# Performance work log

Measured on AMD Instinct MI355X. Metric: run time of the kernel, lower is better.

Reference implementation:

```python
import jax, jax.numpy as jnp
import numpy as np

E = 768       # embed dim
NH = 12       # heads
HD = 64       # head dim
WIN = 14      # window size
DEPTH = 12
PATCH = 16
WINDOW_IDX = (0, 1, 3, 4, 6, 7, 9, 10)
EPS = 1e-6


def layer_norm(x, w, b):
    mu = jnp.mean(x, axis=-1, keepdims=True)
    var = jnp.mean(jnp.square(x - mu), axis=-1, keepdims=True)
    return (x - mu) * jax.lax.rsqrt(var + EPS) * w + b


def get_rel_pos(size, rel_pos):
    # q_size == k_size -> direct lookup, no interpolation
    coords = jnp.arange(size)
    rel = coords[:, None] - coords[None, :] + (size - 1)
    return rel_pos[rel]  # (size, size, HD)


def attention(x, qkv_w, qkv_b, proj_w, proj_b, rel_h, rel_w):
    B, H, W, _ = x.shape
    N = H * W
    qkv = (x.reshape(B, N, E) @ qkv_w + qkv_b).reshape(B, N, 3, NH, HD)
    q = qkv[:, :, 0].transpose(0, 2, 1, 3).reshape(B * NH, N, HD)
    k = qkv[:, :, 1].transpose(0, 2, 1, 3).reshape(B * NH, N, HD)
    v = qkv[:, :, 2].transpose(0, 2, 1, 3).reshape(B * NH, N, HD)
    attn = (q * (HD ** -0.5)) @ k.transpose(0, 2, 1)  # (B*NH, N, N)
    # decomposed relative position bias
    Rh = get_rel_pos(H, rel_h)  # (H, H, HD)
    Rw = get_rel_pos(W, rel_w)  # (W, W, HD)
    r_q = q.reshape(B * NH, H, W, HD)
    rh = jnp.einsum('bhwc,hkc->bhwk', r_q, Rh)
    rw = jnp.einsum('bhwc,wkc->bhwk', r_q, Rw)
    attn = attn.reshape(B * NH, H, W, H, W) + rh[:, :, :, :, None] + rw[:, :, :, None, :]
    attn = jax.nn.softmax(attn.reshape(B * NH, N, N), axis=-1)
    out = (attn @ v).reshape(B, NH, H, W, HD).transpose(0, 2, 3, 1, 4).reshape(B, H, W, E)
    return out @ proj_w + proj_b


def window_partition(x, ws):
    B, H, W, C = x.shape
    pad_h, pad_w = (-H) % ws, (-W) % ws
    x = jnp.pad(x, ((0, 0), (0, pad_h), (0, pad_w), (0, 0)))
    Hp, Wp = H + pad_h, W + pad_w
    x = x.reshape(B, Hp // ws, ws, Wp // ws, ws, C).transpose(0, 1, 3, 2, 4, 5)
    return x.reshape(-1, ws, ws, C), (Hp, Wp)


def window_unpartition(win, ws, pad_hw, hw):
    Hp, Wp = pad_hw
    H, W = hw
    B = win.shape[0] // ((Hp // ws) * (Wp // ws))
    x = win.reshape(B, Hp // ws, Wp // ws, ws, ws, -1).transpose(0, 1, 3, 2, 4, 5)
    return x.reshape(B, Hp, Wp, -1)[:, :H, :W]


def _forward(x, patch_w, patch_b, pos_embed,
             ln1_w, ln1_b, qkv_w, qkv_b, proj_w, proj_b,
             rel_h_win, rel_w_win, rel_h_glob, rel_w_glob,
             ln2_w, ln2_b, fc1_w, fc1_b, fc2_w, fc2_b, out_w, out_b):
    # patch embed: conv 16x16 stride 16
    x = jax.lax.conv_general_dilated(
        x, patch_w, (PATCH, PATCH), 'VALID',
        dimension_numbers=('NCHW', 'OIHW', 'NCHW'))
    x = x.transpose(0, 2, 3, 1) + patch_b  # (B, H, W, C)
    x = x + pos_embed
    win_i, glob_i = 0, 0
    for i in range(DEPTH):
        shortcut = x
        h = layer_norm(x, ln1_w[i], ln1_b[i])
        if i in WINDOW_IDX:
            hw = h.shape[1:3]
            h, pad_hw = window_partition(h, WIN)
            h = attention(h, qkv_w[i], qkv_b[i], proj_w[i], proj_b[i],
                          rel_h_win[win_i], rel_w_win[win_i])
            h = window_unpartition(h, WIN, pad_hw, hw)
            win_i += 1
        else:
            h = attention(h, qkv_w[i], qkv_b[i], proj_w[i], proj_b[i],
                          rel_h_glob[glob_i], rel_w_glob[glob_i])
            glob_i += 1
        x = shortcut + h
        h = layer_norm(x, ln2_w[i], ln2_b[i])
        h = jax.nn.gelu(h @ fc1_w[i] + fc1_b[i], approximate=False) @ fc2_w[i] + fc2_b[i]
        x = x + h
    feat = x.transpose(0, 3, 1, 2)  # (B, C, H, W) == 'last_feat'
    return jnp.einsum('bchw,oc->bohw', feat, out_w) + out_b[None, :, None, None]


def setup_inputs() -> dict:
    key = jax.random.key(0)
    ks = iter(jax.random.split(key, 64))
    def n(shape, s=0.02):
        return jax.random.normal(next(ks), shape, jnp.float32) * s
    B, IMG = 2, 512
    G = IMG // PATCH  # 32
    return {
        'x': jax.random.normal(next(ks), (B, 3, IMG, IMG), jnp.float32),
        'patch_w': n((E, 3, PATCH, PATCH)),
        'patch_b': jnp.zeros((E,), jnp.float32),
        'pos_embed': n((1, G, G, E)),
        'ln1_w': jnp.ones((DEPTH, E), jnp.float32),
        'ln1_b': jnp.zeros((DEPTH, E), jnp.float32),
        'qkv_w': n((DEPTH, E, 3 * E)),
        'qkv_b': jnp.zeros((DEPTH, 3 * E), jnp.float32),
        'proj_w': n((DEPTH, E, E)),
        'proj_b': jnp.zeros((DEPTH, E), jnp.float32),
        'rel_h_win': n((8, 2 * WIN - 1, HD)),
        'rel_w_win': n((8, 2 * WIN - 1, HD)),
        'rel_h_glob': n((4, 2 * G - 1, HD)),
        'rel_w_glob': n((4, 2 * G - 1, HD)),
        'ln2_w': jnp.ones((DEPTH, E), jnp.float32),
        'ln2_b': jnp.zeros((DEPTH, E), jnp.float32),
        'fc1_w': n((DEPTH, E, 4 * E)),
        'fc1_b': jnp.zeros((DEPTH, 4 * E), jnp.float32),
        'fc2_w': n((DEPTH, 4 * E, E)),
        'fc2_b': jnp.zeros((DEPTH, E), jnp.float32),
        'out_w': n((256, E)),
        'out_b': jnp.zeros((256,), jnp.float32),
    }


def reference(x, patch_w, patch_b, pos_embed,
              ln1_w, ln1_b, qkv_w, qkv_b, proj_w, proj_b,
              rel_h_win, rel_w_win, rel_h_glob, rel_w_glob,
              ln2_w, ln2_b, fc1_w, fc1_b, fc2_w, fc2_b, out_w, out_b):
    return _forward(x, patch_w, patch_b, pos_embed,
                    ln1_w, ln1_b, qkv_w, qkv_b, proj_w, proj_b,
                    rel_h_win, rel_w_win, rel_h_glob, rel_w_glob,
                    ln2_w, ln2_b, fc1_w, fc1_b, fc2_w, fc2_b, out_w, out_b)
```

## Files before the change

kernel.cpp:

```cpp
#include <hip/hip_runtime.h>
#include <hip/hip_bf16.h>
#include <math.h>

static constexpr int E   = 768;
static constexpr int NH  = 12;
static constexpr int HD  = 64;
static constexpr int Bsz = 2;
static constexpr int G   = 32;
static constexpr int NTOK = G * G;
static constexpr int ROWS = Bsz * NTOK;
static constexpr int WS  = 14;
static constexpr int NWIN_SIDE = 3;
static constexpr int NWIN = NWIN_SIDE * NWIN_SIDE;
static constexpr int BW  = Bsz * NWIN;
static constexpr int NW  = WS * WS;
static constexpr int WROWS = BW * NW;
static constexpr int WIN_MASK = 0x6DB;

typedef __attribute__((ext_vector_type(8))) short short8;
typedef __attribute__((ext_vector_type(4))) float f32x4;
typedef unsigned short ushort_t;

__device__ __forceinline__ unsigned short f2bf(float x) {
  union { float f; unsigned u; } v; v.f = x;
  unsigned r = v.u + 0x7fffu + ((v.u >> 16) & 1u);
  return (unsigned short)(r >> 16);
}
__device__ __forceinline__ float bf2f(unsigned short h) {
  union { unsigned u; float f; } v; v.u = ((unsigned)h) << 16;
  return v.f;
}

__device__ __forceinline__ void glds16(const void* g, void* l) {
  __builtin_amdgcn_global_load_lds(
      (const __attribute__((address_space(1))) unsigned*)g,
      (__attribute__((address_space(3))) unsigned*)l, 16, 0, 0);
}

__global__ __launch_bounds__(256) void ln_kernel(
    const float* __restrict__ in, const float* __restrict__ w,
    const float* __restrict__ b, ushort_t* __restrict__ out) {
  const int wave = threadIdx.x >> 6, lane = threadIdx.x & 63;
  const int row = blockIdx.x * 4 + wave;
  const float4* r4 = (const float4*)(in + (size_t)row * E);
  float4 v[3];
  v[0] = r4[lane]; v[1] = r4[lane + 64]; v[2] = r4[lane + 128];
  float s = 0.f, s2 = 0.f;
#pragma unroll
  for (int i = 0; i < 3; i++) {
    s += v[i].x + v[i].y + v[i].z + v[i].w;
    s2 += v[i].x * v[i].x + v[i].y * v[i].y + v[i].z * v[i].z + v[i].w * v[i].w;
  }
#pragma unroll
  for (int off = 1; off <= 32; off <<= 1) {
    s += __shfl_xor(s, off);
    s2 += __shfl_xor(s2, off);
  }
  const float mean = s * (1.f / E);
  const float var  = s2 * (1.f / E) - mean * mean;
  const float rs   = rsqrtf(var + 1e-6f);
  ushort_t* o = out + (size_t)row * E;
#pragma unroll
  for (int i = 0; i < 3; i++) {
    const int e0 = (lane + i * 64) * 4;
    ushort4 p;
    p.x = f2bf((v[i].x - mean) * rs * w[e0]     + b[e0]);
    p.y = f2bf((v[i].y - mean) * rs * w[e0 + 1] + b[e0 + 1]);
    p.z = f2bf((v[i].z - mean) * rs * w[e0 + 2] + b[e0 + 2]);
    p.w = f2bf((v[i].w - mean) * rs * w[e0 + 3] + b[e0 + 3]);
    *(ushort4*)&o[e0] = p;
  }
}

enum { OP_QKV = 0, OP_GELU = 1, OP_ADD = 2, OP_POS = 3, OP_HEAD = 4 };

template <int OP, int MAP>
__global__ __launch_bounds__(256) void gemm_bt(
    const ushort_t* __restrict__ A, const ushort_t* __restrict__ Bt,
    const float* __restrict__ bias, const float* __restrict__ res,
    const float* __restrict__ pos, const ushort_t* __restrict__ zbuf,
    void* __restrict__ Cp, int M, int N, int K, int ncol) {
  __shared__ ushort_t As[2][64 * 64];
  __shared__ ushort_t Bs[2][64 * 64];
  const int tid = threadIdx.x, wave = tid >> 6, lane = tid & 63;
  const int lx = lane & 15, ly = lane >> 4;

  const int nwg = gridDim.x;
  const int q = nwg >> 3, r = nwg & 7;
  const int xcd = blockIdx.x & 7, loc = blockIdx.x >> 3;
  const int wgid = ((xcd < r) ? xcd * (q + 1) : r * (q + 1) + (xcd - r) * q) + loc;
  const int brow = wgid / ncol, bcol = wgid - brow * ncol;
  const int row0 = brow * 64, col0 = bcol * 64;
  const int wm = (wave >> 1) * 32, wn = (wave & 1) * 32;
  const int rin = lane >> 3, pseg = lane & 7;
  const int lseg = pseg ^ rin;
  f32x4 acc[2][2] = {};

  const ushort_t* aptr[2];
  const ushort_t* bptr[2];
#pragma unroll
  for (int j = 0; j < 2; j++) {
    const int slot = wave * 2 + j;
    int ar = row0 + slot * 8 + rin;
    if (ar >= M) ar = M - 1;
    if (MAP == 1) {
      const int win = ar / NW, t = ar - win * NW;
      const int wy = t / WS, wx = t - wy * WS;
      const int bI = win / NWIN, wr = win - bI * NWIN;
      const int by = wr / NWIN_SIDE, bx = wr - by * NWIN_SIDE;
      const int y = by * WS + wy, x = bx * WS + wx;
      aptr[j] = (y < G && x < G)
                    ? &A[(((size_t)bI * G + y) * G + x) * E + lseg * 8]
                    : &zbuf[lseg * 8];
    } else if (MAP == 2) {
      const int bI = ar >> 10, t = ar & 1023, y = t >> 5, x = t & 31;
      const int by = y / WS, wy = y - by * WS;
      const int bx = x / WS, wx = x - bx * WS;
      const int win = bI * NWIN + by * NWIN_SIDE + bx;
      aptr[j] = &A[((size_t)win * NW + wy * WS + wx) * E + lseg * 8];
    } else {
      aptr[j] = &A[(size_t)ar * K + lseg * 8];
    }
    const int br = col0 + slot * 8 + rin;
    bptr[j] = &Bt[(size_t)br * K + lseg * 8];
  }

#pragma unroll
  for (int j = 0; j < 2; j++) {
    const int slot = wave * 2 + j;
    glds16(aptr[j], &As[0][slot * 512]);
    glds16(bptr[j], &Bs[0][slot * 512]);
  }
  __syncthreads();

  const int nt = K >> 6;
  int cur = 0;
  for (int t = 0; t < nt; t++) {
    if (t + 1 < nt) {
      const int k1 = (t + 1) << 6;
#pragma unroll
      for (int j = 0; j < 2; j++) {
        const int slot = wave * 2 + j;
        glds16(aptr[j] + k1, &As[cur ^ 1][slot * 512]);
        glds16(bptr[j] + k1, &Bs[cur ^ 1][slot * 512]);
      }
    }
#pragma unroll
    for (int kb = 0; kb < 2; kb++) {
      short8 af[2], bfm[2];
#pragma unroll
      for (int m = 0; m < 2; m++) {
        const int rr = wm + m * 16 + lx;
        af[m] = *(const short8*)&As[cur][rr * 64 + (((kb * 4 + ly) ^ (rr & 7)) * 8)];
      }
#pragma unroll
      for (int n = 0; n < 2; n++) {
        const int rr = wn + n * 16 + lx;
        bfm[n] = *(const short8*)&Bs[cur][rr * 64 + (((kb * 4 + ly) ^ (rr & 7)) * 8)];
      }
      __builtin_amdgcn_s_setprio(1);
#pragma unroll
      for (int m = 0; m < 2; m++)
#pragma unroll
        for (int n = 0; n < 2; n++)
          acc[m][n] = __builtin_amdgcn_mfma_f32_16x16x32_bf16(af[m], bfm[n], acc[m][n], 0, 0, 0);
      __builtin_amdgcn_s_setprio(0);
    }
    __syncthreads();
    cur ^= 1;
  }

#pragma unroll
  for (int m = 0; m < 2; m++) {
#pragma unroll
    for (int r4 = 0; r4 < 4; r4++) {
      const int gr = row0 + wm + m * 16 + ly * 4 + r4;
      if (gr >= M) continue;
#pragma unroll
      for (int n = 0; n < 2; n++) {
        const int gc = col0 + wn + n * 16 + lx;
        float v = acc[m][n][r4] + bias[gc];
        if (OP == OP_GELU) v = 0.5f * v * (1.f + erff(v * 0.70710678118654752f));
        if (OP == OP_ADD)  v += res[(size_t)gr * N + gc];
        if (OP == OP_POS)  v += pos[(size_t)(gr & 1023) * N + gc];
        if (OP == OP_QKV || OP == OP_GELU)
          ((ushort_t*)Cp)[(size_t)gr * N + gc] = f2bf(v);
        else if (OP == OP_HEAD)
          ((float*)Cp)[(((size_t)(gr >> 10) * 256 + gc) << 10) | (gr & 1023)] = v;
        else
          ((float*)Cp)[(size_t)gr * N + gc] = v;
      }
    }
  }
}

__global__ __launch_bounds__(128) void attn_mfma(
    const ushort_t* __restrict__ qkv, ushort_t* __restrict__ out,
    const float* __restrict__ relh, const float* __restrict__ relw,
    int Hd, int Wd) {
  const int Ntok = Hd * Wd;
  __shared__ ushort_t smem[11392];
  ushort_t* Ks   = smem;
  ushort_t* Vst  = smem + 2048;
  ushort_t* Ps   = smem + 4608;
  ushort_t* Qs   = smem;
  ushort_t* RelS = smem + 2048;
  ushort_t* Th   = smem + 6144;
  ushort_t* Tw   = smem + 8256;
  ushort_t* khw  = smem + 10368;

  const int tid = threadIdx.x, wave = tid >> 6, lane = tid & 63;
  const int lx = lane & 15, ly = lane >> 4;
  const int bh = blockIdx.y, b = bh / NH, nh = bh % NH;
  const int q0 = blockIdx.x * 32;
  const size_t base = (size_t)b * Ntok * 2304 + nh * 64;

#pragma unroll
  for (int i = 0; i < 2; i++) {
    const int fv = i * 128 + tid;
    const int row = fv >> 3, dv8 = (fv & 7) * 8;
    const int qq = q0 + row;
    short8 v = {};
    if (qq < Ntok) v = *(const short8*)&qkv[base + (size_t)qq * 2304 + dv8];
    *(short8*)&Qs[(row * 64 + dv8) ^ ((row & 7) << 3)] = v;
  }
  for (int k = tid; k < 1024; k += 128) {
    const int kc = min(k, Ntok - 1);
    const int kh = kc / Wd;
    khw[k] = (ushort_t)((kh << 8) | (kc - kh * Wd));
  }
  __syncthreads();

  short8 qa[2];
  {
    const int row = wave * 16 + lx;
#pragma unroll
    for (int kb = 0; kb < 2; kb++)
      qa[kb] = *(const short8*)&Qs[(row * 64 + kb * 32 + ly * 8) ^ ((row & 7) << 3)];
  }
  int qh_r[4], qw_r[4];
#pragma unroll
  for (int r = 0; r < 4; r++) {
    const int qq = q0 + wave * 16 + ly * 4 + r;
    const int qc = min(qq, Ntok - 1);
    qh_r[r] = qc / Wd;
    qw_r[r] = qc - qh_r[r] * Wd;
  }

  for (int t = 0; t < 2; t++) {
    const float* rel = t ? relw : relh;
    const int TR = t ? (2 * Wd - 1) : (2 * Hd - 1);
    __syncthreads();
#pragma unroll
    for (int i = 0; i < 4; i++) {
      const int fv = i * 128 + tid;
      const int row = fv >> 3, c8 = (fv & 7) * 8;
      short8 v = {};
      if (row < TR) {
        const float* rp = &rel[(size_t)row * 64 + c8];
        const float4 a = *(const float4*)rp;
        const float4 bq = *(const float4*)(rp + 4);
        v[0] = (short)f2bf(a.x);  v[1] = (short)f2bf(a.y);
        v[2] = (short)f2bf(a.z);  v[3] = (short)f2bf(a.w);
        v[4] = (short)f2bf(bq.x); v[5] = (short)f2bf(bq.y);
        v[6] = (short)f2bf(bq.z); v[7] = (short)f2bf(bq.w);
      }
      *(short8*)&RelS[(row * 64 + c8) ^ ((row & 7) << 3)] = v;
    }
    __syncthreads();
    const int NT = (TR + 15) >> 4;
    ushort_t* T = t ? Tw : Th;
    for (int nt = 0; nt < NT; nt++) {
      f32x4 a = {};
      __builtin_amdgcn_s_setprio(1);
#pragma unroll
      for (int kb = 0; kb < 2; kb++) {
        const int rrow = nt * 16 + lx;
        short8 bfv = *(const short8*)&RelS[(rrow * 64 + kb * 32 + ly * 8) ^ ((rrow & 7) << 3)];
        a = __builtin_amdgcn_mfma_f32_16x16x32_bf16(qa[kb], bfv, a, 0, 0, 0);
      }
      __builtin_amdgcn_s_setprio(0);
#pragma unroll
      for (int reg = 0; reg < 4; reg++)
        T[(wave * 16 + ly * 4 + reg) * 66 + nt * 16 + lx] = f2bf(a[reg]);
    }
  }

  f32x4 o[4] = {};
  float m_[4], l_[4];
#pragma unroll
  for (int r = 0; r < 4; r++) { m_[r] = -3e38f; l_[r] = 0.f; }

  const int nkt = (Ntok + 31) >> 5;
  const int srow = tid >> 3, c7 = tid & 7, dv8s = c7 * 8;
  const int vswz = (c7 & 3) << 3;

  short8 kpre[2], vpre[2];
#pragma unroll
  for (int i = 0; i < 2; i++) {
    const int gk = srow + i * 16;
    short8 kv = {}, vv = {};
    if (gk < Ntok) {
      kv = *(const short8*)&qkv[base + 768 + (size_t)gk * 2304 + dv8s];
      vv = *(const short8*)&qkv[base + 1536 + (size_t)gk * 2304 + dv8s];
    }
    kpre[i] = kv; vpre[i] = vv;
  }

  for (int kt = 0; kt < nkt; kt++) {
    __syncthreads();
#pragma unroll
    for (int i = 0; i < 2; i++) {
      const int row = srow + i * 16;
      *(short8*)&Ks[(row * 64 + dv8s) ^ ((row & 7) << 3)] = kpre[i];
      const int kcol = row ^ vswz;
#pragma unroll
      for (int j = 0; j < 8; j++)
        Vst[(dv8s + j) * 40 + kcol] = (ushort_t)vpre[i][j];
    }
    if (kt + 1 < nkt) {
#pragma unroll
      for (int i = 0; i < 2; i++) {
        const int gk = (kt + 1) * 32 + srow + i * 16;
        short8 kv = {}, vv = {};
        if (gk < Ntok) {
          kv = *(const short8*)&qkv[base + 768 + (size_t)gk * 2304 + dv8s];
          vv = *(const short8*)&qkv[base + 1536 + (size_t)gk * 2304 + dv8s];
        }
        kpre[i] = kv; vpre[i] = vv;
      }
    }
    __syncthreads();

    f32x4 c[2] = {};
    __builtin_amdgcn_s_setprio(1);
#pragma unroll
    for (int kb = 0; kb < 2; kb++)
#pragma unroll
      for (int ct = 0; ct < 2; ct++) {
        const int krow = ct * 16 + lx;
        short8 kf = *(const short8*)&Ks[(krow * 64 + kb * 32 + ly * 8) ^ ((krow & 7) << 3)];
        c[ct] = __builtin_amdgcn_mfma_f32_16x16x32_bf16(qa[kb], kf, c[ct], 0, 0, 0);
      }
    __builtin_amdgcn_s_setprio(0);

    const int k0a = kt * 32 + lx, k1a = k0a + 16;
    const int tv0 = khw[k0a], tv1 = khw[k1a];
    const int kh0 = tv0 >> 8, kw0 = tv0 & 255;
    const int kh1 = tv1 >> 8, kw1 = tv1 & 255;
    float pv0[4], pv1[4], mt[4];
#pragma unroll
    for (int r = 0; r < 4; r++) {
      const int trow = (wave * 16 + ly * 4 + r) * 66;
      float s0 = c[0][r] * 0.125f + bf2f(Th[trow + qh_r[r] - kh0 + Hd - 1])
               + bf2f(Tw[trow + qw_r[r] - kw0 + Wd - 1]);
      float s1 = c[1][r] * 0.125f + bf2f(Th[trow + qh_r[r] - kh1 + Hd - 1])
               + bf2f(Tw[trow + qw_r[r] - kw1 + Wd - 1]);
      if (k0a >= Ntok) s0 = -1e30f;
      if (k1a >= Ntok) s1 = -1e30f;
      pv0[r] = s0; pv1[r] = s1;
      mt[r] = fmaxf(s0, s1);
    }
    const float dmax = fmaxf(fmaxf(mt[0] - m_[0], mt[1] - m_[1]),
                             fmaxf(mt[2] - m_[2], mt[3] - m_[3]));
    if (!__all(dmax <= 8.f)) {
#pragma unroll
      for (int r = 0; r < 4; r++) {
        float mr = mt[r];
#pragma unroll
        for (int off = 1; off <= 8; off <<= 1) mr = fmaxf(mr, __shfl_xor(mr, off));
        const float mn = fmaxf(m_[r], mr);
        const float sc = __expf(m_[r] - mn);
        m_[r] = mn; l_[r] *= sc;
#pragma unroll
        for (int dt = 0; dt < 4; dt++) o[dt][r] *= sc;
      }
    }
#pragma unroll
    for (int r = 0; r < 4; r++) {
      const float p0 = __expf(pv0[r] - m_[r]);
      const float p1 = __expf(pv1[r] - m_[r]);
      l_[r] += p0 + p1;
      const int pb = wave * 640 + (ly * 4 + r) * 40;
      Ps[pb + lx]      = f2bf(p0);
      Ps[pb + 16 + lx] = f2bf(p1);
    }
    short8 pf = *(const short8*)&Ps[wave * 640 + lx * 40 + ly * 8];
    __builtin_amdgcn_s_setprio(1);
#pragma unroll
    for (int dt = 0; dt < 4; dt++) {
      const int drow = dt * 16 + lx;
      short8 vf = *(const short8*)&Vst[drow * 40 + ((ly * 8) ^ (((drow >> 3) & 3) << 3))];
      o[dt] = __builtin_amdgcn_mfma_f32_16x16x32_bf16(pf, vf, o[dt], 0, 0, 0);
    }
    __builtin_amdgcn_s_setprio(0);
  }

#pragma unroll
  for (int r = 0; r < 4; r++) {
#pragma unroll
    for (int off = 1; off <= 8; off <<= 1) l_[r] += __shfl_xor(l_[r], off);
    const int qq = q0 + wave * 16 + ly * 4 + r;
    if (qq >= Ntok) continue;
    const float inv = 1.f / l_[r];
#pragma unroll
    for (int dt = 0; dt < 4; dt++)
      out[((size_t)b * Ntok + qq) * E + nh * 64 + dt * 16 + lx] = f2bf(o[dt][r] * inv);
  }
}

__global__ __launch_bounds__(256) void im2col(const float* __restrict__ x,
                                              ushort_t* __restrict__ out) {
  const int blk = blockIdx.x;
  const int b = blk >> 10, t = blk & 1023, gy = t >> 5, gx = t & 31;
  for (int k = threadIdx.x; k < 768; k += 256) {
    const int ci = k >> 8, rem = k & 255, py = rem >> 4, px = rem & 15;
    out[(size_t)blk * 768 + k] =
        f2bf(x[(((size_t)b * 3 + ci) * 512 + gy * 16 + py) * 512 + gx * 16 + px]);
  }
}

__global__ __launch_bounds__(256) void prep_wt(
    const float* __restrict__ qkvw, const float* __restrict__ projw,
    const float* __restrict__ fc1w, const float* __restrict__ fc2w,
    ushort_t* __restrict__ wq, ushort_t* __restrict__ wp,
    ushort_t* __restrict__ w1, ushort_t* __restrict__ w2) {
  __shared__ float tile[32][33];
  const int blk = blockIdx.x;
  const float* W; ushort_t* Wt; int Kd, Nd, tn, tk;
  if (blk < 1728)      { W = qkvw;  Wt = wq; Kd = 768;  Nd = 2304; tn = blk % 72;          tk = blk / 72; }
  else if (blk < 2304) { W = projw; Wt = wp; Kd = 768;  Nd = 768;  tn = (blk - 1728) % 24; tk = (blk - 1728) / 24; }
  else if (blk < 4608) { W = fc1w;  Wt = w1; Kd = 768;  Nd = 3072; tn = (blk - 2304) % 96; tk = (blk - 2304) / 96; }
  else                 { W = fc2w;  Wt = w2; Kd = 3072; Nd = 768;  tn = (blk - 4608) % 24; tk = (blk - 4608) / 24; }
  const int k0 = tk * 32, n0 = tn * 32;
  const int c = threadIdx.x & 31, r8 = threadIdx.x >> 5;
#pragma unroll
  for (int i = 0; i < 4; i++) {
    const int kr = i * 8 + r8;
    tile[kr][c] = W[(size_t)(k0 + kr) * Nd + n0 + c];
  }
  __syncthreads();
#pragma unroll
  for (int i = 0; i < 4; i++) {
    const int nr = i * 8 + r8;
    Wt[(size_t)(n0 + nr) * Kd + k0 + c] = f2bf(tile[c][nr]);
  }
}

__global__ __launch_bounds__(256) void cast_bf16(const float* __restrict__ in,
                                                 ushort_t* __restrict__ out, int n) {
  const int idx = (blockIdx.x * 256 + threadIdx.x) * 4;
  if (idx + 3 < n) {
    const float4 v = *(const float4*)&in[idx];
    ushort4 p;
    p.x = f2bf(v.x); p.y = f2bf(v.y); p.z = f2bf(v.z); p.w = f2bf(v.w);
    *(ushort4*)&out[idx] = p;
  }
}

__global__ __launch_bounds__(256) void zinit(ushort_t* __restrict__ z) {
  z[blockIdx.x * 256 + threadIdx.x] = 0;
}

extern "C" void kernel_launch(void* const* d_in, const int* in_sizes, int n_in,
                              void* d_out, int out_size, void* d_ws, size_t ws_size,
                              hipStream_t stream) {
  const float* x_in     = (const float*)d_in[0];
  const float* patch_w  = (const float*)d_in[1];
  const float* patch_b  = (const float*)d_in[2];
  const float* pos_emb  = (const float*)d_in[3];
  const float* ln1_w    = (const float*)d_in[4];
  const float* ln1_b    = (const float*)d_in[5];
  const float* qkv_w    = (const float*)d_in[6];
  const float* qkv_b    = (const float*)d_in[7];
  const float* proj_w   = (const float*)d_in[8];
  const float* proj_b   = (const float*)d_in[9];
  const float* rel_h_w  = (const float*)d_in[10];
  const float* rel_w_w  = (const float*)d_in[11];
  const float* rel_h_g  = (const float*)d_in[12];
  const float* rel_w_g  = (const float*)d_in[13];
  const float* ln2_w    = (const float*)d_in[14];
  const float* ln2_b    = (const float*)d_in[15];
  const float* fc1_w    = (const float*)d_in[16];
  const float* fc1_b    = (const float*)d_in[17];
  const float* fc2_w    = (const float*)d_in[18];
  const float* fc2_b    = (const float*)d_in[19];
  const float* out_w    = (const float*)d_in[20];
  const float* out_b    = (const float*)d_in[21];
  float* outp = (float*)d_out;

  float* xbuf = (float*)d_ws;
  ushort_t* hb16    = (ushort_t*)(xbuf + (size_t)ROWS * E);
  ushort_t* qkv16   = hb16 + (size_t)ROWS * E;
  ushort_t* attnw16 = qkv16 + (size_t)WROWS * 3 * E;
  ushort_t* wtbuf   = attnw16 + (size_t)WROWS * E;
  ushort_t* wq = wtbuf;
  ushort_t* wp = wq + 2304 * 768;
  ushort_t* w1 = wp + 768 * 768;
  ushort_t* w2 = w1 + 3072 * 768;
  ushort_t* zbuf = wtbuf + (size_t)9216 * 768;
  ushort_t* imb16 = hb16;
  ushort_t* h1b16 = qkv16;
  ushort_t* pwT16 = wtbuf;
  ushort_t* headW16 = wtbuf;

  zinit<<<4, 256, 0, stream>>>(zbuf);

  cast_bf16<<<576, 256, 0, stream>>>(patch_w, pwT16, 768 * 768);
  im2col<<<ROWS, 256, 0, stream>>>(x_in, imb16);
  gemm_bt<OP_POS, 0><<<12 * 32, 256, 0, stream>>>(
      imb16, pwT16, patch_b, nullptr, pos_emb, nullptr, xbuf, ROWS, E, E, 12);

  int win_i = 0, glob_i = 0;
  for (int i = 0; i < 12; i++) {
    const bool is_win = (WIN_MASK >> i) & 1;

    prep_wt<<<6912, 256, 0, stream>>>(
        qkv_w + (size_t)i * E * 3 * E, proj_w + (size_t)i * E * E,
        fc1_w + (size_t)i * E * 4 * E, fc2_w + (size_t)i * 4 * E * E,
        wq, wp, w1, w2);

    ln_kernel<<<ROWS / 4, 256, 0, stream>>>(xbuf, ln1_w + i * E, ln1_b + i * E, hb16);

    if (is_win) {
      gemm_bt<OP_QKV, 1><<<36 * 56, 256, 0, stream>>>(
          hb16, wq, qkv_b + i * 3 * E, nullptr, nullptr, zbuf, qkv16,
          WROWS, 3 * E, E, 36);
      attn_mfma<<<dim3(7, BW * NH), 128, 0, stream>>>(
          qkv16, attnw16, rel_h_w + (size_t)win_i * (2 * WS - 1) * HD,
          rel_w_w + (size_t)win_i * (2 * WS - 1) * HD, WS, WS);
      win_i++;
    } else {
      gemm_bt<OP_QKV, 0><<<36 * 32, 256, 0, stream>>>(
          hb16, wq, qkv_b + i * 3 * E, nullptr, nullptr, nullptr, qkv16,
          ROWS, 3 * E, E, 36);
      attn_mfma<<<dim3(32, Bsz * NH), 128, 0, stream>>>(
          qkv16, attnw16, rel_h_g + (size_t)glob_i * (2 * G - 1) * HD,
          rel_w_g + (size_t)glob_i * (2 * G - 1) * HD, G, G);
      glob_i++;
    }

    if (is_win)
      gemm_bt<OP_ADD, 2><<<12 * 32, 256, 0, stream>>>(
          attnw16, wp, proj_b + i * E, xbuf, nullptr, nullptr, xbuf,
          ROWS, E, E, 12);
    else
      gemm_bt<OP_ADD, 0><<<12 * 32, 256, 0, stream>>>(
          attnw16, wp, proj_b + i * E, xbuf, nullptr, nullptr, xbuf,
          ROWS, E, E, 12);

    ln_kernel<<<ROWS / 4, 256, 0, stream>>>(xbuf, ln2_w + i * E, ln2_b + i * E, hb16);
    gemm_bt<OP_GELU, 0><<<48 * 32, 256, 0, stream>>>(
        hb16, w1, fc1_b + i * 4 * E, nullptr, nullptr, nullptr, h1b16,
        ROWS, 4 * E, E, 48);
    gemm_bt<OP_ADD, 0><<<12 * 32, 256, 0, stream>>>(
        h1b16, w2, fc2_b + i * E, xbuf, nullptr, nullptr, xbuf,
        ROWS, E, 4 * E, 12);
  }

  cast_bf16<<<192, 256, 0, stream>>>(out_w, headW16, 256 * 768);
  cast_bf16<<<1536, 256, 0, stream>>>(xbuf, hb16, ROWS * E);
  gemm_bt<OP_HEAD, 0><<<4 * 32, 256, 0, stream>>>(
      hb16, headW16, out_b, nullptr, nullptr, nullptr, outp, ROWS, 256, E, 4);
}
```

Baseline: 1.834 ms.

## Run QKV GEMM on unpadded tokens and gather windows inside attention; batch weight prep

```diff
diff --git a/kernel.cpp b/kernel.cpp
--- a/kernel.cpp
+++ b/kernel.cpp
@@ -14,7 +14,6 @@
 static constexpr int NWIN = NWIN_SIDE * NWIN_SIDE;
 static constexpr int BW  = Bsz * NWIN;
 static constexpr int NW  = WS * WS;
-static constexpr int WROWS = BW * NW;
 static constexpr int WIN_MASK = 0x6DB;
 
 typedef __attribute__((ext_vector_type(8))) short short8;
@@ -74,12 +73,12 @@
 
 enum { OP_QKV = 0, OP_GELU = 1, OP_ADD = 2, OP_POS = 3, OP_HEAD = 4 };
 
-template <int OP, int MAP>
+template <int OP>
 __global__ __launch_bounds__(256) void gemm_bt(
     const ushort_t* __restrict__ A, const ushort_t* __restrict__ Bt,
     const float* __restrict__ bias, const float* __restrict__ res,
-    const float* __restrict__ pos, const ushort_t* __restrict__ zbuf,
-    void* __restrict__ Cp, int M, int N, int K, int ncol) {
+    const float* __restrict__ pos, void* __restrict__ Cp,
+    int M, int N, int K, int ncol) {
   __shared__ ushort_t As[2][64 * 64];
   __shared__ ushort_t Bs[2][64 * 64];
   const int tid = threadIdx.x, wave = tid >> 6, lane = tid & 63;
@@ -103,24 +102,7 @@
     const int slot = wave * 2 + j;
     int ar = row0 + slot * 8 + rin;
     if (ar >= M) ar = M - 1;
-    if (MAP == 1) {
-      const int win = ar / NW, t = ar - win * NW;
-      const int wy = t / WS, wx = t - wy * WS;
-      const int bI = win / NWIN, wr = win - bI * NWIN;
-      const int by = wr / NWIN_SIDE, bx = wr - by * NWIN_SIDE;
-      const int y = by * WS + wy, x = bx * WS + wx;
-      aptr[j] = (y < G && x < G)
-                    ? &A[(((size_t)bI * G + y) * G + x) * E + lseg * 8]
-                    : &zbuf[lseg * 8];
-    } else if (MAP == 2) {
-      const int bI = ar >> 10, t = ar & 1023, y = t >> 5, x = t & 31;
-      const int by = y / WS, wy = y - by * WS;
-      const int bx = x / WS, wx = x - bx * WS;
-      const int win = bI * NWIN + by * NWIN_SIDE + bx;
-      aptr[j] = &A[((size_t)win * NW + wy * WS + wx) * E + lseg * 8];
-    } else {
-      aptr[j] = &A[(size_t)ar * K + lseg * 8];
-    }
+    aptr[j] = &A[(size_t)ar * K + lseg * 8];
     const int br = col0 + slot * 8 + rin;
     bptr[j] = &Bt[(size_t)br * K + lseg * 8];
   }
@@ -194,10 +176,11 @@
   }
 }
 
+template <int WIN>
 __global__ __launch_bounds__(128) void attn_mfma(
     const ushort_t* __restrict__ qkv, ushort_t* __restrict__ out,
     const float* __restrict__ relh, const float* __restrict__ relw,
-    int Hd, int Wd) {
+    const float* __restrict__ qkvb, int Hd, int Wd) {
   const int Ntok = Hd * Wd;
   __shared__ ushort_t smem[11392];
   ushort_t* Ks   = smem;
@@ -211,17 +194,34 @@
 
   const int tid = threadIdx.x, wave = tid >> 6, lane = tid & 63;
   const int lx = lane & 15, ly = lane >> 4;
-  const int bh = blockIdx.y, b = bh / NH, nh = bh % NH;
+  const int bh = blockIdx.y;
+  const int nh = bh % NH;
+  int b, by = 0, bx = 0;
+  if (WIN) {
+    const int wb = bh / NH;
+    b = wb / NWIN;
+    const int wr = wb - b * NWIN;
+    by = wr / NWIN_SIDE; bx = wr - by * NWIN_SIDE;
+  } else {
+    b = bh / NH;
+  }
   const int q0 = blockIdx.x * 32;
-  const size_t base = (size_t)b * Ntok * 2304 + nh * 64;
+  const size_t base = (size_t)b * NTOK * 2304 + nh * 64;
 
 #pragma unroll
   for (int i = 0; i < 2; i++) {
     const int fv = i * 128 + tid;
     const int row = fv >> 3, dv8 = (fv & 7) * 8;
-    const int qq = q0 + row;
-    short8 v = {};
-    if (qq < Ntok) v = *(const short8*)&qkv[base + (size_t)qq * 2304 + dv8];
+    const int j2 = min(q0 + row, Ntok - 1);
+    size_t addr;
+    if (WIN) {
+      const int qh = (j2 * 2341) >> 15, qw = j2 - qh * 14;
+      const int gy = min(by * 14 + qh, G - 1), gx = min(bx * 14 + qw, G - 1);
+      addr = base + (size_t)(gy * G + gx) * 2304 + dv8;
+    } else {
+      addr = base + (size_t)j2 * 2304 + dv8;
+    }
+    short8 v = *(const short8*)&qkv[addr];
     *(short8*)&Qs[(row * 64 + dv8) ^ ((row & 7) << 3)] = v;
   }
   for (int k = tid; k < 1024; k += 128) {
@@ -241,8 +241,7 @@
   int qh_r[4], qw_r[4];
 #pragma unroll
   for (int r = 0; r < 4; r++) {
-    const int qq = q0 + wave * 16 + ly * 4 + r;
-    const int qc = min(qq, Ntok - 1);
+    const int qc = min(q0 + wave * 16 + ly * 4 + r, Ntok - 1);
     qh_r[r] = qc / Wd;
     qw_r[r] = qc - qh_r[r] * Wd;
   }
@@ -295,17 +294,37 @@
   const int srow = tid >> 3, c7 = tid & 7, dv8s = c7 * 8;
   const int vswz = (c7 & 3) << 3;
 
+  short8 kb8 = {}, vb8 = {};
+  if (WIN) {
+#pragma unroll
+    for (int j = 0; j < 8; j++) {
+      kb8[j] = (short)f2bf(qkvb[768 + nh * 64 + dv8s + j]);
+      vb8[j] = (short)f2bf(qkvb[1536 + nh * 64 + dv8s + j]);
+    }
+  }
+
+  auto load_kv = [&](int gk, short8& kv, short8& vv) {
+    kv = short8{}; vv = short8{};
+    if (gk < Ntok) {
+      if (WIN) {
+        const int kh = (gk * 2341) >> 15, kw = gk - kh * 14;
+        const int gy = by * 14 + kh, gx = bx * 14 + kw;
+        if (gy < G && gx < G) {
+          const size_t a = base + (size_t)(gy * G + gx) * 2304;
+          kv = *(const short8*)&qkv[a + 768 + dv8s];
+          vv = *(const short8*)&qkv[a + 1536 + dv8s];
+        } else { kv = kb8; vv = vb8; }
+      } else {
+        const size_t a = base + (size_t)gk * 2304;
+        kv = *(const short8*)&qkv[a + 768 + dv8s];
+        vv = *(const short8*)&qkv[a + 1536 + dv8s];
+      }
+    }
+  };
+
   short8 kpre[2], vpre[2];
 #pragma unroll
-  for (int i = 0; i < 2; i++) {
-    const int gk = srow + i * 16;
-    short8 kv = {}, vv = {};
-    if (gk < Ntok) {
-      kv = *(const short8*)&qkv[base + 768 + (size_t)gk * 2304 + dv8s];
-      vv = *(const short8*)&qkv[base + 1536 + (size_t)gk * 2304 + dv8s];
-    }
-    kpre[i] = kv; vpre[i] = vv;
-  }
+  for (int i = 0; i < 2; i++) load_kv(srow + i * 16, kpre[i], vpre[i]);
 
   for (int kt = 0; kt < nkt; kt++) {
     __syncthreads();
@@ -320,15 +339,8 @@
     }
     if (kt + 1 < nkt) {
 #pragma unroll
-      for (int i = 0; i < 2; i++) {
-        const int gk = (kt + 1) * 32 + srow + i * 16;
-        short8 kv = {}, vv = {};
-        if (gk < Ntok) {
-          kv = *(const short8*)&qkv[base + 768 + (size_t)gk * 2304 + dv8s];
-          vv = *(const short8*)&qkv[base + 1536 + (size_t)gk * 2304 + dv8s];
-        }
-        kpre[i] = kv; vpre[i] = vv;
-      }
+      for (int i = 0; i < 2; i++)
+        load_kv((kt + 1) * 32 + srow + i * 16, kpre[i], vpre[i]);
     }
     __syncthreads();
 
@@ -402,10 +414,18 @@
     for (int off = 1; off <= 8; off <<= 1) l_[r] += __shfl_xor(l_[r], off);
     const int qq = q0 + wave * 16 + ly * 4 + r;
     if (qq >= Ntok) continue;
+    int orow;
+    if (WIN) {
+      const int gy = by * 14 + qh_r[r], gx = bx * 14 + qw_r[r];
+      if (gy >= G || gx >= G) continue;
+      orow = b * NTOK + gy * G + gx;
+    } else {
+      orow = b * NTOK + qq;
+    }
     const float inv = 1.f / l_[r];
 #pragma unroll
     for (int dt = 0; dt < 4; dt++)
-      out[((size_t)b * Ntok + qq) * E + nh * 64 + dt * 16 + lx] = f2bf(o[dt][r] * inv);
+      out[(size_t)orow * E + nh * 64 + dt * 16 + lx] = f2bf(o[dt][r] * inv);
   }
 }
 
@@ -420,18 +440,23 @@
   }
 }
 
-__global__ __launch_bounds__(256) void prep_wt(
+__global__ __launch_bounds__(256) void prep_wt_all(
     const float* __restrict__ qkvw, const float* __restrict__ projw,
     const float* __restrict__ fc1w, const float* __restrict__ fc2w,
     ushort_t* __restrict__ wq, ushort_t* __restrict__ wp,
     ushort_t* __restrict__ w1, ushort_t* __restrict__ w2) {
   __shared__ float tile[32][33];
-  const int blk = blockIdx.x;
+  int blk = blockIdx.x;
+  const int l = blk / 6912; blk -= l * 6912;
   const float* W; ushort_t* Wt; int Kd, Nd, tn, tk;
-  if (blk < 1728)      { W = qkvw;  Wt = wq; Kd = 768;  Nd = 2304; tn = blk % 72;          tk = blk / 72; }
-  else if (blk < 2304) { W = projw; Wt = wp; Kd = 768;  Nd = 768;  tn = (blk - 1728) % 24; tk = (blk - 1728) / 24; }
-  else if (blk < 4608) { W = fc1w;  Wt = w1; Kd = 768;  Nd = 3072; tn = (blk - 2304) % 96; tk = (blk - 2304) / 96; }
-  else                 { W = fc2w;  Wt = w2; Kd = 3072; Nd = 768;  tn = (blk - 4608) % 24; tk = (blk - 4608) / 24; }
+  if (blk < 1728)      { W = qkvw + (size_t)l * 768 * 2304;  Wt = wq + (size_t)l * 2304 * 768;
+                         Kd = 768;  Nd = 2304; tn = blk % 72;          tk = blk / 72; }
+  else if (blk < 2304) { W = projw + (size_t)l * 768 * 768;  Wt = wp + (size_t)l * 768 * 768;
+                         Kd = 768;  Nd = 768;  tn = (blk - 1728) % 24; tk = (blk - 1728) / 24; }
+  else if (blk < 4608) { W = fc1w + (size_t)l * 768 * 3072;  Wt = w1 + (size_t)l * 3072 * 768;
+                         Kd = 768;  Nd = 3072; tn = (blk - 2304) % 96; tk = (blk - 2304) / 96; }
+  else                 { W = fc2w + (size_t)l * 3072 * 768;  Wt = w2 + (size_t)l * 768 * 3072;
+                         Kd = 3072; Nd = 768;  tn = (blk - 4608) % 24; tk = (blk - 4608) / 24; }
   const int k0 = tk * 32, n0 = tn * 32;
   const int c = threadIdx.x & 31, r8 = threadIdx.x >> 5;
 #pragma unroll
@@ -456,10 +481,6 @@
     p.x = f2bf(v.x); p.y = f2bf(v.y); p.z = f2bf(v.z); p.w = f2bf(v.w);
     *(ushort4*)&out[idx] = p;
   }
-}
-
-__global__ __launch_bounds__(256) void zinit(ushort_t* __restrict__ z) {
-  z[blockIdx.x * 256 + threadIdx.x] = 0;
 }
 
 extern "C" void kernel_launch(void* const* d_in, const int* in_sizes, int n_in,
@@ -492,74 +513,61 @@
   float* xbuf = (float*)d_ws;
   ushort_t* hb16    = (ushort_t*)(xbuf + (size_t)ROWS * E);
   ushort_t* qkv16   = hb16 + (size_t)ROWS * E;
-  ushort_t* attnw16 = qkv16 + (size_t)WROWS * 3 * E;
-  ushort_t* wtbuf   = attnw16 + (size_t)WROWS * E;
-  ushort_t* wq = wtbuf;
-  ushort_t* wp = wq + 2304 * 768;
-  ushort_t* w1 = wp + 768 * 768;
-  ushort_t* w2 = w1 + 3072 * 768;
-  ushort_t* zbuf = wtbuf + (size_t)9216 * 768;
+  ushort_t* attnw16 = qkv16 + (size_t)ROWS * 3 * E;
+  ushort_t* h1b16   = attnw16 + (size_t)ROWS * E;
+  ushort_t* wqAll   = h1b16 + (size_t)ROWS * 4 * E;
+  ushort_t* wpAll   = wqAll + (size_t)12 * 2304 * 768;
+  ushort_t* w1All   = wpAll + (size_t)12 * 768 * 768;
+  ushort_t* w2All   = w1All + (size_t)12 * 3072 * 768;
+  ushort_t* pwT16   = w2All + (size_t)12 * 768 * 3072;
+  ushort_t* headW16 = pwT16 + (size_t)768 * 768;
   ushort_t* imb16 = hb16;
-  ushort_t* h1b16 = qkv16;
-  ushort_t* pwT16 = wtbuf;
-  ushort_t* headW16 = wtbuf;
-
-  zinit<<<4, 256, 0, stream>>>(zbuf);
-
+
+  prep_wt_all<<<12 * 6912, 256, 0, stream>>>(qkv_w, proj_w, fc1_w, fc2_w,
+                                             wqAll, wpAll, w1All, w2All);
   cast_bf16<<<576, 256, 0, stream>>>(patch_w, pwT16, 768 * 768);
+  cast_bf16<<<192, 256, 0, stream>>>(out_w, headW16, 256 * 768);
+
   im2col<<<ROWS, 256, 0, stream>>>(x_in, imb16);
-  gemm_bt<OP_POS, 0><<<12 * 32, 256, 0, stream>>>(
-      imb16, pwT16, patch_b, nullptr, pos_emb, nullptr, xbuf, ROWS, E, E, 12);
+  gemm_bt<OP_POS><<<12 * 32, 256, 0, stream>>>(
+      imb16, pwT16, patch_b, nullptr, pos_emb, xbuf, ROWS, E, E, 12);
 
   int win_i = 0, glob_i = 0;
   for (int i = 0; i < 12; i++) {
     const bool is_win = (WIN_MASK >> i) & 1;
-
-    prep_wt<<<6912, 256, 0, stream>>>(
-        qkv_w + (size_t)i * E * 3 * E, proj_w + (size_t)i * E * E,
-        fc1_w + (size_t)i * E * 4 * E, fc2_w + (size_t)i * 4 * E * E,
-        wq, wp, w1, w2);
+    const ushort_t* wq = wqAll + (size_t)i * 2304 * 768;
+    const ushort_t* wp = wpAll + (size_t)i * 768 * 768;
+    const ushort_t* w1 = w1All + (size_t)i * 3072 * 768;
+    const ushort_t* w2 = w2All + (size_t)i * 768 * 3072;
 
     ln_kernel<<<ROWS / 4, 256, 0, stream>>>(xbuf, ln1_w + i * E, ln1_b + i * E, hb16);
 
+    gemm_bt<OP_QKV><<<36 * 32, 256, 0, stream>>>(
+        hb16, wq, qkv_b + i * 3 * E, nullptr, nullptr, qkv16, ROWS, 3 * E, E, 36);
+
     if (is_win) {
-      gemm_bt<OP_QKV, 1><<<36 * 56, 256, 0, stream>>>(
-          hb16, wq, qkv_b + i * 3 * E, nullptr, nullptr, zbuf, qkv16,
-          WROWS, 3 * E, E, 36);
-      attn_mfma<<<dim3(7, BW * NH), 128, 0, stream>>>(
+      attn_mfma<1><<<dim3(7, BW * NH), 128, 0, stream>>>(
           qkv16, attnw16, rel_h_w + (size_t)win_i * (2 * WS - 1) * HD,
-          rel_w_w + (size_t)win_i * (2 * WS - 1) * HD, WS, WS);
+          rel_w_w + (size_t)win_i * (2 * WS - 1) * HD, qkv_b + i * 3 * E, WS, WS);
       win_i++;
     } else {
-      gemm_bt<OP_QKV, 0><<<36 * 32, 256, 0, stream>>>(
-          hb16, wq, qkv_b + i * 3 * E, nullptr, nullptr, nullptr, qkv16,
-          ROWS, 3 * E, E, 36);
-      attn_mfma<<<dim3(32, Bsz * NH), 128, 0, stream>>>(
+      attn_mfma<0><<<dim3(32, Bsz * NH), 128, 0, stream>>>(
           qkv16, attnw16, rel_h_g + (size_t)glob_i * (2 * G - 1) * HD,
-          rel_w_g + (size_t)glob_i * (2 * G - 1) * HD, G, G);
+          rel_w_g + (size_t)glob_i * (2 * G - 1) * HD, qkv_b + i * 3 * E, G, G);
       glob_i++;
     }
 
-    if (is_win)
-      gemm_bt<OP_ADD, 2><<<12 * 32, 256, 0, stream>>>(
-          attnw16, wp, proj_b + i * E, xbuf, nullptr, nullptr, xbuf,
-          ROWS, E, E, 12);
-    else
-      gemm_bt<OP_ADD, 0><<<12 * 32, 256, 0, stream>>>(
-          attnw16, wp, proj_b + i * E, xbuf, nullptr, nullptr, xbuf,
-          ROWS, E, E, 12);
+    gemm_bt<OP_ADD><<<12 * 32, 256, 0, stream>>>(
+        attnw16, wp, proj_b + i * E, xbuf, nullptr, xbuf, ROWS, E, E, 12);
 
     ln_kernel<<<ROWS / 4, 256, 0, stream>>>(xbuf, ln2_w + i * E, ln2_b + i * E, hb16);
-    gemm_bt<OP_GELU, 0><<<48 * 32, 256, 0, stream>>>(
-        hb16, w1, fc1_b + i * 4 * E, nullptr, nullptr, nullptr, h1b16,
-        ROWS, 4 * E, E, 48);
-    gemm_bt<OP_ADD, 0><<<12 * 32, 256, 0, stream>>>(
-        h1b16, w2, fc2_b + i * E, xbuf, nullptr, nullptr, xbuf,
-        ROWS, E, 4 * E, 12);
-  }
-
-  cast_bf16<<<192, 256, 0, stream>>>(out_w, headW16, 256 * 768);
+    gemm_bt<OP_GELU><<<48 * 32, 256, 0, stream>>>(
+        hb16, w1, fc1_b + i * 4 * E, nullptr, nullptr, h1b16, ROWS, 4 * E, E, 48);
+    gemm_bt<OP_ADD><<<12 * 32, 256, 0, stream>>>(
+        h1b16, w2, fc2_b + i * E, xbuf, nullptr, xbuf, ROWS, E, 4 * E, 12);
+  }
+
   cast_bf16<<<1536, 256, 0, stream>>>(xbuf, hb16, ROWS * E);
-  gemm_bt<OP_HEAD, 0><<<4 * 32, 256, 0, stream>>>(
-      hb16, headW16, out_b, nullptr, nullptr, nullptr, outp, ROWS, 256, E, 4);
-}
+  gemm_bt<OP_HEAD><<<4 * 32, 256, 0, stream>>>(
+      hb16, headW16, out_b, nullptr, nullptr, outp, ROWS, 256, E, 4);
+}
```

New measurement: 1.937 ms. +5.6%, slower.

## Compute QKV on unpadded image rows then gather into windows; widen weight transpose tiles

Applied to the files above, without the earlier changes.

```diff
diff --git a/kernel.cpp b/kernel.cpp
--- a/kernel.cpp
+++ b/kernel.cpp
@@ -78,8 +78,8 @@
 __global__ __launch_bounds__(256) void gemm_bt(
     const ushort_t* __restrict__ A, const ushort_t* __restrict__ Bt,
     const float* __restrict__ bias, const float* __restrict__ res,
-    const float* __restrict__ pos, const ushort_t* __restrict__ zbuf,
-    void* __restrict__ Cp, int M, int N, int K, int ncol) {
+    const float* __restrict__ pos, void* __restrict__ Cp,
+    int M, int N, int K, int ncol) {
   __shared__ ushort_t As[2][64 * 64];
   __shared__ ushort_t Bs[2][64 * 64];
   const int tid = threadIdx.x, wave = tid >> 6, lane = tid & 63;
@@ -103,16 +103,7 @@
     const int slot = wave * 2 + j;
     int ar = row0 + slot * 8 + rin;
     if (ar >= M) ar = M - 1;
-    if (MAP == 1) {
-      const int win = ar / NW, t = ar - win * NW;
-      const int wy = t / WS, wx = t - wy * WS;
-      const int bI = win / NWIN, wr = win - bI * NWIN;
-      const int by = wr / NWIN_SIDE, bx = wr - by * NWIN_SIDE;
-      const int y = by * WS + wy, x = bx * WS + wx;
-      aptr[j] = (y < G && x < G)
-                    ? &A[(((size_t)bI * G + y) * G + x) * E + lseg * 8]
-                    : &zbuf[lseg * 8];
-    } else if (MAP == 2) {
+    if (MAP == 2) {
       const int bI = ar >> 10, t = ar & 1023, y = t >> 5, x = t & 31;
       const int by = y / WS, wy = y - by * WS;
       const int bx = x / WS, wx = x - bx * WS;
@@ -219,9 +210,8 @@
   for (int i = 0; i < 2; i++) {
     const int fv = i * 128 + tid;
     const int row = fv >> 3, dv8 = (fv & 7) * 8;
-    const int qq = q0 + row;
-    short8 v = {};
-    if (qq < Ntok) v = *(const short8*)&qkv[base + (size_t)qq * 2304 + dv8];
+    const int qq = min(q0 + row, Ntok - 1);
+    short8 v = *(const short8*)&qkv[base + (size_t)qq * 2304 + dv8];
     *(short8*)&Qs[(row * 64 + dv8) ^ ((row & 7) << 3)] = v;
   }
   for (int k = tid; k < 1024; k += 128) {
@@ -241,8 +231,7 @@
   int qh_r[4], qw_r[4];
 #pragma unroll
   for (int r = 0; r < 4; r++) {
-    const int qq = q0 + wave * 16 + ly * 4 + r;
-    const int qc = min(qq, Ntok - 1);
+    const int qc = min(q0 + wave * 16 + ly * 4 + r, Ntok - 1);
     qh_r[r] = qc / Wd;
     qw_r[r] = qc - qh_r[r] * Wd;
   }
@@ -409,6 +398,29 @@
   }
 }
 
+__global__ __launch_bounds__(128) void qkv_winpart(
+    const ushort_t* __restrict__ qi, const float* __restrict__ qkvb,
+    ushort_t* __restrict__ qw) {
+  const int row = blockIdx.x;
+  const int win = row / NW, t = row - win * NW;
+  const int wy = t / WS, wx = t - wy * WS;
+  const int b = win / NWIN, wr = win - b * NWIN;
+  const int by = wr / NWIN_SIDE, bx = wr - by * NWIN_SIDE;
+  const int y = by * WS + wy, x = bx * WS + wx;
+  short8* dst = (short8*)(qw + (size_t)row * 2304);
+  if (y < G && x < G) {
+    const short8* src = (const short8*)(qi + (((size_t)b * G + y) * G + x) * 2304);
+    for (int e = threadIdx.x; e < 288; e += 128) dst[e] = src[e];
+  } else {
+    for (int e = threadIdx.x; e < 288; e += 128) {
+      short8 v;
+#pragma unroll
+      for (int j = 0; j < 8; j++) v[j] = (short)f2bf(qkvb[e * 8 + j]);
+      dst[e] = v;
+    }
+  }
+}
+
 __global__ __launch_bounds__(256) void im2col(const float* __restrict__ x,
                                               ushort_t* __restrict__ out) {
   const int blk = blockIdx.x;
@@ -420,31 +432,39 @@
   }
 }
 
-__global__ __launch_bounds__(256) void prep_wt(
+__global__ __launch_bounds__(256) void prep_wt64(
     const float* __restrict__ qkvw, const float* __restrict__ projw,
     const float* __restrict__ fc1w, const float* __restrict__ fc2w,
     ushort_t* __restrict__ wq, ushort_t* __restrict__ wp,
     ushort_t* __restrict__ w1, ushort_t* __restrict__ w2) {
-  __shared__ float tile[32][33];
+  __shared__ float tile[64][65];
   const int blk = blockIdx.x;
   const float* W; ushort_t* Wt; int Kd, Nd, tn, tk;
-  if (blk < 1728)      { W = qkvw;  Wt = wq; Kd = 768;  Nd = 2304; tn = blk % 72;          tk = blk / 72; }
-  else if (blk < 2304) { W = projw; Wt = wp; Kd = 768;  Nd = 768;  tn = (blk - 1728) % 24; tk = (blk - 1728) / 24; }
-  else if (blk < 4608) { W = fc1w;  Wt = w1; Kd = 768;  Nd = 3072; tn = (blk - 2304) % 96; tk = (blk - 2304) / 96; }
-  else                 { W = fc2w;  Wt = w2; Kd = 3072; Nd = 768;  tn = (blk - 4608) % 24; tk = (blk - 4608) / 24; }
-  const int k0 = tk * 32, n0 = tn * 32;
-  const int c = threadIdx.x & 31, r8 = threadIdx.x >> 5;
-#pragma unroll
-  for (int i = 0; i < 4; i++) {
-    const int kr = i * 8 + r8;
-    tile[kr][c] = W[(size_t)(k0 + kr) * Nd + n0 + c];
+  if (blk < 432)       { W = qkvw;  Wt = wq; Kd = 768;  Nd = 2304; tn = blk % 36;          tk = blk / 36; }
+  else if (blk < 576)  { W = projw; Wt = wp; Kd = 768;  Nd = 768;  tn = (blk - 432) % 12;  tk = (blk - 432) / 12; }
+  else if (blk < 1152) { W = fc1w;  Wt = w1; Kd = 768;  Nd = 3072; tn = (blk - 576) % 48;  tk = (blk - 576) / 48; }
+  else                 { W = fc2w;  Wt = w2; Kd = 3072; Nd = 768;  tn = (blk - 1152) % 12; tk = (blk - 1152) / 12; }
+  const int k0 = tk * 64, n0 = tn * 64;
+  const int kr = threadIdx.x >> 2, cg = (threadIdx.x & 3) * 16;
+  const float* src = &W[(size_t)(k0 + kr) * Nd + n0 + cg];
+#pragma unroll
+  for (int j = 0; j < 4; j++) {
+    const float4 v = *(const float4*)&src[j * 4];
+    tile[kr][cg + j * 4 + 0] = v.x;
+    tile[kr][cg + j * 4 + 1] = v.y;
+    tile[kr][cg + j * 4 + 2] = v.z;
+    tile[kr][cg + j * 4 + 3] = v.w;
   }
   __syncthreads();
-#pragma unroll
-  for (int i = 0; i < 4; i++) {
-    const int nr = i * 8 + r8;
-    Wt[(size_t)(n0 + nr) * Kd + k0 + c] = f2bf(tile[c][nr]);
-  }
+  const int nr = kr;
+  short8 o0, o1;
+#pragma unroll
+  for (int j = 0; j < 8; j++) o0[j] = (short)f2bf(tile[cg + j][nr]);
+#pragma unroll
+  for (int j = 0; j < 8; j++) o1[j] = (short)f2bf(tile[cg + 8 + j][nr]);
+  ushort_t* dst = &Wt[(size_t)(n0 + nr) * Kd + k0 + cg];
+  *(short8*)&dst[0] = o0;
+  *(short8*)&dst[8] = o1;
 }
 
 __global__ __launch_bounds__(256) void cast_bf16(const float* __restrict__ in,
@@ -456,10 +476,6 @@
     p.x = f2bf(v.x); p.y = f2bf(v.y); p.z = f2bf(v.z); p.w = f2bf(v.w);
     *(ushort4*)&out[idx] = p;
   }
-}
-
-__global__ __launch_bounds__(256) void zinit(ushort_t* __restrict__ z) {
-  z[blockIdx.x * 256 + threadIdx.x] = 0;
 }
 
 extern "C" void kernel_launch(void* const* d_in, const int* in_sizes, int n_in,
@@ -491,75 +507,64 @@
 
   float* xbuf = (float*)d_ws;
   ushort_t* hb16    = (ushort_t*)(xbuf + (size_t)ROWS * E);
-  ushort_t* qkv16   = hb16 + (size_t)ROWS * E;
-  ushort_t* attnw16 = qkv16 + (size_t)WROWS * 3 * E;
-  ushort_t* wtbuf   = attnw16 + (size_t)WROWS * E;
-  ushort_t* wq = wtbuf;
-  ushort_t* wp = wq + 2304 * 768;
-  ushort_t* w1 = wp + 768 * 768;
-  ushort_t* w2 = w1 + 3072 * 768;
-  ushort_t* zbuf = wtbuf + (size_t)9216 * 768;
+  ushort_t* qkvimg  = hb16 + (size_t)ROWS * E;
+  ushort_t* qkvwin  = qkvimg + (size_t)ROWS * 3 * E;
+  ushort_t* attnw16 = qkvwin + (size_t)WROWS * 3 * E;
+  ushort_t* h1b16   = attnw16 + (size_t)WROWS * E;
+  ushort_t* wq      = h1b16 + (size_t)ROWS * 4 * E;
+  ushort_t* wp      = wq + (size_t)2304 * 768;
+  ushort_t* w1      = wp + (size_t)768 * 768;
+  ushort_t* w2      = w1 + (size_t)3072 * 768;
+  ushort_t* pwT16   = w2 + (size_t)768 * 3072;
+  ushort_t* headW16 = pwT16 + (size_t)768 * 768;
   ushort_t* imb16 = hb16;
-  ushort_t* h1b16 = qkv16;
-  ushort_t* pwT16 = wtbuf;
-  ushort_t* headW16 = wtbuf;
-
-  zinit<<<4, 256, 0, stream>>>(zbuf);
 
   cast_bf16<<<576, 256, 0, stream>>>(patch_w, pwT16, 768 * 768);
+  cast_bf16<<<192, 256, 0, stream>>>(out_w, headW16, 256 * 768);
+
   im2col<<<ROWS, 256, 0, stream>>>(x_in, imb16);
   gemm_bt<OP_POS, 0><<<12 * 32, 256, 0, stream>>>(
-      imb16, pwT16, patch_b, nullptr, pos_emb, nullptr, xbuf, ROWS, E, E, 12);
+      imb16, pwT16, patch_b, nullptr, pos_emb, xbuf, ROWS, E, E, 12);
 
   int win_i = 0, glob_i = 0;
   for (int i = 0; i < 12; i++) {
     const bool is_win = (WIN_MASK >> i) & 1;
 
-    prep_wt<<<6912, 256, 0, stream>>>(
+    prep_wt64<<<1728, 256, 0, stream>>>(
         qkv_w + (size_t)i * E * 3 * E, proj_w + (size_t)i * E * E,
         fc1_w + (size_t)i * E * 4 * E, fc2_w + (size_t)i * 4 * E * E,
         wq, wp, w1, w2);
 
     ln_kernel<<<ROWS / 4, 256, 0, stream>>>(xbuf, ln1_w + i * E, ln1_b + i * E, hb16);
 
+    gemm_bt<OP_QKV, 0><<<36 * 32, 256, 0, stream>>>(
+        hb16, wq, qkv_b + i * 3 * E, nullptr, nullptr, qkvimg, ROWS, 3 * E, E, 36);
+
     if (is_win) {
-      gemm_bt<OP_QKV, 1><<<36 * 56, 256, 0, stream>>>(
-          hb16, wq, qkv_b + i * 3 * E, nullptr, nullptr, zbuf, qkv16,
-          WROWS, 3 * E, E, 36);
+      qkv_winpart<<<WROWS, 128, 0, stream>>>(qkvimg, qkv_b + i * 3 * E, qkvwin);
       attn_mfma<<<dim3(7, BW * NH), 128, 0, stream>>>(
-          qkv16, attnw16, rel_h_w + (size_t)win_i * (2 * WS - 1) * HD,
+          qkvwin, attnw16, rel_h_w + (size_t)win_i * (2 * WS - 1) * HD,
           rel_w_w + (size_t)win_i * (2 * WS - 1) * HD, WS, WS);
       win_i++;
+      gemm_bt<OP_ADD, 2><<<12 * 32, 256, 0, stream>>>(
+          attnw16, wp, proj_b + i * E, xbuf, nullptr, xbuf, ROWS, E, E, 12);
     } else {
-      gemm_bt<OP_QKV, 0><<<36 * 32, 256, 0, stream>>>(
-          hb16, wq, qkv_b + i * 3 * E, nullptr, nullptr, nullptr, qkv16,
-          ROWS, 3 * E, E, 36);
       attn_mfma<<<dim3(32, Bsz * NH), 128, 0, stream>>>(
-          qkv16, attnw16, rel_h_g + (size_t)glob_i * (2 * G - 1) * HD,
+          qkvimg, attnw16, rel_h_g + (size_t)glob_i * (2 * G - 1) * HD,
           rel_w_g + (size_t)glob_i * (2 * G - 1) * HD, G, G);
       glob_i++;
-    }
-
-    if (is_win)
-      gemm_bt<OP_ADD, 2><<<12 * 32, 256, 0, stream>>>(
-          attnw16, wp, proj_b + i * E, xbuf, nullptr, nullptr, xbuf,
-          ROWS, E, E, 12);
-    else
       gemm_bt<OP_ADD, 0><<<12 * 32, 256, 0, stream>>>(
-          attnw16, wp, proj_b + i * E, xbuf, nullptr, nullptr, xbuf,
-          ROWS, E, E, 12);
+          attnw16, wp, proj_b + i * E, xbuf, nullptr, xbuf, ROWS, E, E, 12);
+    }
 
     ln_kernel<<<ROWS / 4, 256, 0, stream>>>(xbuf, ln2_w + i * E, ln2_b + i * E, hb16);
     gemm_bt<OP_GELU, 0><<<48 * 32, 256, 0, stream>>>(
-        hb16, w1, fc1_b + i * 4 * E, nullptr, nullptr, nullptr, h1b16,
-        ROWS, 4 * E, E, 48);
+        hb16, w1, fc1_b + i * 4 * E, nullptr, nullptr, h1b16, ROWS, 4 * E, E, 48);
     gemm_bt<OP_ADD, 0><<<12 * 32, 256, 0, stream>>>(
-        h1b16, w2, fc2_b + i * E, xbuf, nullptr, nullptr, xbuf,
-        ROWS, E, 4 * E, 12);
-  }
-
-  cast_bf16<<<192, 256, 0, stream>>>(out_w, headW16, 256 * 768);
+        h1b16, w2, fc2_b + i * E, xbuf, nullptr, xbuf, ROWS, E, 4 * E, 12);
+  }
+
   cast_bf16<<<1536, 256, 0, stream>>>(xbuf, hb16, ROWS * E);
   gemm_bt<OP_HEAD, 0><<<4 * 32, 256, 0, stream>>>(
-      hb16, headW16, out_b, nullptr, nullptr, nullptr, outp, ROWS, 256, E, 4);
-}
+      hb16, headW16, out_b, nullptr, nullptr, outp, ROWS, 256, E, 4);
+}
```

Result: no change. 1.842 ms (+0.4%).
